# Optimization experiments

Measured on AMD Instinct MI355X. Metric: run time of the kernel, lower is better.

Reference implementation:

```python
import jax, jax.numpy as jnp
import numpy as np

VOCAB = 50000
OOV = 1000
EMB = 256
H = 512          # decoder hidden
ENC = 512        # 2 * encoder_hidden (bidirectional)
B, S, T = 32, 256, 8
NEG = -1e20


def setup_inputs() -> dict:
    key = jax.random.key(0)
    ks = jax.random.split(key, 16)
    inp = {
        'dec_x': jax.random.randint(ks[0], (B, T), 0, VOCAB),
        'enc_x_with_oov': jax.random.randint(ks[1], (B, S), 0, VOCAB + OOV),
        'enc_len': jax.random.randint(ks[2], (B,), 64, S + 1),
        'enc_output': jax.random.normal(ks[3], (B, S, ENC), jnp.float32),
        'enc_h': jax.random.normal(ks[4], (B, H), jnp.float32),
        'enc_c': jax.random.normal(ks[5], (B, H), jnp.float32),
        'batch_size': B,
        'dec_len': T,
        # learned parameters
        'embedding': jax.random.normal(ks[6], (VOCAB, EMB), jnp.float32) * 0.02,
        'lstm_k': jax.random.normal(ks[7], (EMB, 4 * H), jnp.float32) * 0.02,
        'lstm_r': jax.random.normal(ks[8], (H, 4 * H), jnp.float32) * 0.02,
        'lstm_b': jnp.zeros((4 * H,), jnp.float32),
        'attn_w': jax.random.normal(ks[9], (H, ENC), jnp.float32) * 0.02,
        'out_w': jax.random.normal(ks[10], (ENC + H, H), jnp.float32) * 0.02,
        'out_b': jnp.zeros((H,), jnp.float32),
        'gen_w': jax.random.normal(ks[11], (H, VOCAB), jnp.float32) * 0.02,
        'copy_w': jax.random.normal(ks[12], (ENC, H), jnp.float32) * 0.02,
        'copy_b': jnp.zeros((H,), jnp.float32),
    }
    return inp


def _lstm(x, h0, c0, Wk, Wr, b):
    # x: [B, T, E] -> hidden states [B, T, H], final (h, c)
    def step(carry, x_t):
        h, c = carry
        z = x_t @ Wk + h @ Wr + b  # [B, 4H]
        i, f, g, o = jnp.split(z, 4, axis=-1)
        c = jax.nn.sigmoid(f) * c + jax.nn.sigmoid(i) * jnp.tanh(g)
        h = jax.nn.sigmoid(o) * jnp.tanh(c)
        return (h, c), h
    (h, c), hs = jax.lax.scan(step, (h0, c0), jnp.swapaxes(x, 0, 1))
    return jnp.swapaxes(hs, 0, 1), h, c


def reference(dec_x, enc_x_with_oov, enc_len, enc_output, enc_h, enc_c,
              batch_size, dec_len, embedding, lstm_k, lstm_r, lstm_b,
              attn_w, out_w, out_b, gen_w, copy_w, copy_b):
    mask = jnp.arange(S) < enc_len[:, None]          # [B, S] True = keep

    embed_dec = embedding[dec_x]                      # [B, T, E]
    hidden, state_h, state_c = _lstm(embed_dec, enc_h, enc_c, lstm_k, lstm_r, lstm_b)

    # attention ('general' score)
    q = hidden @ attn_w                               # [B, T, ENC]
    scores = jnp.einsum('bte,bse->bts', q, enc_output)
    scores = jnp.where(mask[:, None, :], scores, NEG)
    attn = jax.nn.softmax(scores, axis=2)             # [B, T, S]
    context = jnp.einsum('bts,bse->bte', attn, enc_output)
    attn_out = jnp.tanh(jnp.concatenate([context, hidden], axis=-1) @ out_w + out_b)  # [B, T, H]

    # generation scores, padded with tiny constant for OOV slots
    gen = jnp.exp(attn_out @ gen_w)                   # [B, T, VOCAB]
    gen = jnp.pad(gen, ((0, 0), (0, 0), (0, OOV)), constant_values=1e-10)

    # copy scores scattered into extended vocab
    k = jnp.tanh(enc_output @ copy_w + copy_b)        # [B, S, H]
    cs = jnp.einsum('bsh,bth->bts', k, attn_out)      # [B, T, S]
    cs = jnp.exp(jnp.where(mask[:, None, :], cs, NEG))
    Vt = VOCAB + OOV
    copy_vocab = jnp.zeros((B, T, Vt), cs.dtype).at[
        jnp.arange(B)[:, None, None],
        jnp.arange(T)[None, :, None],
        enc_x_with_oov[:, None, :],
    ].add(cs)                                         # scatter-add, dup indices sum

    total = gen + copy_vocab
    total_prob = jnp.log(total / jnp.sum(total, axis=2, keepdims=True))
    return total_prob, state_h, state_c
```

## Files before the change

kernel.cpp:

```cpp
#include <hip/hip_runtime.h>
#include <hip/hip_bf16.h>

typedef unsigned short u16;
typedef unsigned int   u32;
typedef __attribute__((ext_vector_type(4))) float f4v;
typedef __attribute__((ext_vector_type(8))) short s8v;
typedef __attribute__((ext_vector_type(4))) unsigned int u4v;

#define NB   32
#define NS   256
#define NT   8
#define NH   512
#define NENC 512
#define NEMB 256
#define NVOC 50000
#define NVT  51000

__device__ __forceinline__ float bf2f(u16 u){ return __uint_as_float(((u32)u)<<16); }
__device__ __forceinline__ u16 f2bf(float f){
  u32 x = __float_as_uint(f);
  return (u16)((x + 0x7fffu + ((x>>16)&1u)) >> 16);
}
__device__ __forceinline__ s8v ld_frag16(const u16* p){
  union{ s8v v; u4v u; } t;
  t.u = *(const u4v*)p;
  return t.v;
}
__device__ __forceinline__ f4v mfma16(s8v a, s8v b, f4v c){
  return __builtin_amdgcn_mfma_f32_16x16x32_bf16(a,b,c,0,0,0);
}
__device__ __forceinline__ float sigm(float x){ return 1.f/(1.f+__expf(-x)); }

__global__ __launch_bounds__(256)
void transpose_cvt(const float* __restrict__ in, u16* __restrict__ out,
                   int K, int N)
{
  __shared__ u16 tile[32*40];
  const int n0 = blockIdx.x*32, k0 = blockIdx.y*32;
  const int tid = threadIdx.x;
  {
    int r = tid>>3, c4 = tid&7;
    int c = n0 + c4*4;
    if (c+4 > N) c = N-4;
    f4v v = *(const f4v*)(in + (size_t)(k0+r)*N + c);
    uint2 p;
    p.x = (u32)f2bf(v.x) | ((u32)f2bf(v.y)<<16);
    p.y = (u32)f2bf(v.z) | ((u32)f2bf(v.w)<<16);
    *(uint2*)&tile[r*40 + c4*4] = p;
  }
  __syncthreads();
  {
    int r2 = tid>>3, kc = tid&7;
    int n = n0 + r2;
    if (n < N){
      u16 e[4];
      #pragma unroll
      for (int j=0; j<4; ++j) e[j] = tile[(kc*4+j)*40 + r2];
      *(uint2*)(out + (size_t)n*K + k0 + kc*4) = *(uint2*)e;
    }
  }
}

__global__ __launch_bounds__(256)
void cvt_bf16(const float* __restrict__ src, u16* __restrict__ dst){
  int i = (blockIdx.x*256 + threadIdx.x) * 4;
  f4v v = *(const f4v*)(src + i);
  uint2 p;
  p.x = (u32)f2bf(v.x) | ((u32)f2bf(v.y)<<16);
  p.y = (u32)f2bf(v.z) | ((u32)f2bf(v.w)<<16);
  *(uint2*)(dst + i) = p;
}

template<int BM, int BN, int EPI, bool ABF16, bool AGATHER, bool MXA>
__global__ __launch_bounds__(256)
void gemm_bt(const void* __restrict__ Av, const u16* __restrict__ Bt,
             float* __restrict__ C, const int* __restrict__ a_idx,
             const float* __restrict__ bias, float* __restrict__ rowsum,
             int K, int lda, int ldc, int nlim)
{
  constexpr int LDT = 40;
  constexpr int PA  = ABF16 ? BM/64 : BM/32;
  constexpr int PB  = BN/64;
  __shared__ u16 Al[2][BM*LDT];
  __shared__ u16 Bl[2][BN*LDT];
  const int tid  = threadIdx.x;
  const int lane = tid & 63;
  const int wave = tid >> 6;
  const int m0 = (MXA ? blockIdx.x : blockIdx.y) * BM;
  const int n0 = (MXA ? blockIdx.y : blockIdx.x) * BN;
  constexpr int TM = BM/32;
  constexpr int TN = BN/32;
  const int wm = (wave>>1)*(BM/2);
  const int wn = (wave&1)*(BN/2);
  const int q  = lane >> 4;
  const int ln = lane & 15;

  const u16*  aS16[PA];
  const float* aS32[PA];
  int aOff[PA];
  if (ABF16){
    const u16* Ag = (const u16*)Av;
    #pragma unroll
    for (int p=0; p<PA; ++p){
      int el = tid + p*256, row = el>>2, ck = el&3;
      aS16[p] = Ag + (size_t)(m0+row)*lda + ck*8;
      aS32[p] = nullptr;
      aOff[p] = row*LDT + ck*8;
    }
  } else {
    const float* Ag = (const float*)Av;
    #pragma unroll
    for (int p=0; p<PA; ++p){
      int el = tid + p*256, row = el>>3, ck = el&7;
      int grow = AGATHER ? a_idx[m0+row] : (m0+row);
      aS32[p] = Ag + (size_t)grow*lda + ck*4;
      aS16[p] = nullptr;
      aOff[p] = row*LDT + ck*4;
    }
  }
  const u16* bS[PB];
  int bOff[PB];
  #pragma unroll
  for (int p=0; p<PB; ++p){
    int el = tid + p*256, row = el>>2, ck = el&3;
    int nr = n0 + row; if (nr >= nlim) nr = nlim-1;
    bS[p]   = Bt + (size_t)nr*K + ck*8;
    bOff[p] = row*LDT + ck*8;
  }

  f4v acc[TM][TN];
  #pragma unroll
  for (int im=0; im<TM; ++im)
    #pragma unroll
    for (int in=0; in<TN; ++in) acc[im][in] = 0.f;

  u4v aR[PA]; f4v aF[PA]; u4v bR[PB];
  if (ABF16){
    #pragma unroll
    for (int p=0; p<PA; ++p) aR[p] = *(const u4v*)(aS16[p]);
  } else {
    #pragma unroll
    for (int p=0; p<PA; ++p) aF[p] = *(const f4v*)(aS32[p]);
  }
  #pragma unroll
  for (int p=0; p<PB; ++p) bR[p] = *(const u4v*)(bS[p]);

  const int KB = K >> 5;
  int cur = 0;
  for (int kb=0; kb<KB; ++kb){
    if (ABF16){
      #pragma unroll
      for (int p=0; p<PA; ++p) *(u4v*)&Al[cur][aOff[p]] = aR[p];
    } else {
      #pragma unroll
      for (int p=0; p<PA; ++p){
        uint2 pk;
        pk.x = (u32)f2bf(aF[p].x) | ((u32)f2bf(aF[p].y)<<16);
        pk.y = (u32)f2bf(aF[p].z) | ((u32)f2bf(aF[p].w)<<16);
        *(uint2*)&Al[cur][aOff[p]] = pk;
      }
    }
    #pragma unroll
    for (int p=0; p<PB; ++p) *(u4v*)&Bl[cur][bOff[p]] = bR[p];
    if (kb+1 < KB){
      const int ko = (kb+1)*32;
      if (ABF16){
        #pragma unroll
        for (int p=0; p<PA; ++p) aR[p] = *(const u4v*)(aS16[p] + ko);
      } else {
        #pragma unroll
        for (int p=0; p<PA; ++p) aF[p] = *(const f4v*)(aS32[p] + ko);
      }
      #pragma unroll
      for (int p=0; p<PB; ++p) bR[p] = *(const u4v*)(bS[p] + ko);
    }
    __syncthreads();
    s8v af[TM], bfr[TN];
    #pragma unroll
    for (int im=0; im<TM; ++im)
      af[im] = ld_frag16(&Al[cur][(wm+im*16+ln)*LDT + q*8]);
    #pragma unroll
    for (int in=0; in<TN; ++in)
      bfr[in] = ld_frag16(&Bl[cur][(wn+in*16+ln)*LDT + q*8]);
    #pragma unroll
    for (int im=0; im<TM; ++im)
      #pragma unroll
      for (int in=0; in<TN; ++in)
        acc[im][in] = mfma16(af[im], bfr[in], acc[im][in]);
    cur ^= 1;
  }

  #pragma unroll
  for (int im=0; im<TM; ++im){
    const int rbase = m0 + wm + im*16 + q*4;
    #pragma unroll
    for (int in=0; in<TN; ++in){
      const int col = n0 + wn + in*16 + ln;
      if (EPI == 0){
        #pragma unroll
        for (int r=0; r<4; ++r)
          C[(size_t)(rbase+r)*ldc + col] = acc[im][in][r];
      } else if (EPI == 1){
        float bb = bias[col];
        u16* Cb = (u16*)C;
        #pragma unroll
        for (int r=0; r<4; ++r)
          Cb[(size_t)(rbase+r)*ldc + col] = f2bf(tanhf(acc[im][in][r] + bb));
      }
    }
  }
}

__global__ __launch_bounds__(256, 3)
void gen_nat(const u16* __restrict__ A,
             const float* __restrict__ W,
             float* __restrict__ outp)
{
  constexpr int LDT = 40;
  __shared__ u16 Al[2][256*LDT];
  __shared__ u16 Bl[2][64*LDT];
  const int tid  = threadIdx.x;
  const int lane = tid & 63, wave = tid >> 6;
  const int q = lane >> 4, ln = lane & 15;
  const int wm = (wave >> 1) * 128;
  const int wn = (wave & 1) * 32;
  const int n0 = blockIdx.x * 64;

  const int arow = tid >> 2, ack = (tid & 3) * 8;
  const int kp = tid >> 4;
  const int nw = tid & 15;
  int bcol = n0 + nw*4; if (bcol > NVOC-4) bcol = NVOC-4;
  const float* w0 = W + (size_t)(2*kp)  *NVOC + bcol;
  const float* w1 = W + (size_t)(2*kp+1)*NVOC + bcol;
  const int bLoff = (nw*4)*LDT + kp*2;
  const size_t CH = (size_t)32*NVOC;

  f4v acc[8][2];
  #pragma unroll
  for (int im=0; im<8; ++im){ acc[im][0] = 0.f; acc[im][1] = 0.f; }

  u4v aA[4], aB[4];
  f4v b0A, b1A, b0B, b1B;
  #pragma unroll
  for (int p=0; p<4; ++p)
    aA[p] = *(const u4v*)(A + (size_t)(arow + p*64)*NH + ack);
  b0A = *(const f4v*)(w0);
  b1A = *(const f4v*)(w1);
  #pragma unroll
  for (int p=0; p<4; ++p)
    aB[p] = *(const u4v*)(A + (size_t)(arow + p*64)*NH + 32 + ack);
  b0B = *(const f4v*)(w0 + CH);
  b1B = *(const f4v*)(w1 + CH);

  for (int kb=0; kb<16; kb+=2){
    #pragma unroll
    for (int p=0; p<4; ++p) *(u4v*)&Al[0][(arow + p*64)*LDT + ack] = aA[p];
    #pragma unroll
    for (int i=0; i<4; ++i){
      u32 v = (u32)f2bf(b0A[i]) | ((u32)f2bf(b1A[i])<<16);
      *(u32*)&Bl[0][bLoff + i*LDT] = v;
    }
    if (kb+2 < 16){
      #pragma unroll
      for (int p=0; p<4; ++p)
        aA[p] = *(const u4v*)(A + (size_t)(arow + p*64)*NH + (kb+2)*32 + ack);
      b0A = *(const f4v*)(w0 + (size_t)(kb+2)*CH);
      b1A = *(const f4v*)(w1 + (size_t)(kb+2)*CH);
    }
    __syncthreads();
    {
      s8v bf0 = ld_frag16(&Bl[0][(wn + ln)*LDT + q*8]);
      s8v bf1 = ld_frag16(&Bl[0][(wn + 16 + ln)*LDT + q*8]);
      #pragma unroll
      for (int im=0; im<8; ++im){
        s8v af = ld_frag16(&Al[0][(wm + im*16 + ln)*LDT + q*8]);
        acc[im][0] = mfma16(af, bf0, acc[im][0]);
        acc[im][1] = mfma16(af, bf1, acc[im][1]);
      }
    }
    #pragma unroll
    for (int p=0; p<4; ++p) *(u4v*)&Al[1][(arow + p*64)*LDT + ack] = aB[p];
    #pragma unroll
    for (int i=0; i<4; ++i){
      u32 v = (u32)f2bf(b0B[i]) | ((u32)f2bf(b1B[i])<<16);
      *(u32*)&Bl[1][bLoff + i*LDT] = v;
    }
    if (kb+3 < 16){
      #pragma unroll
      for (int p=0; p<4; ++p)
        aB[p] = *(const u4v*)(A + (size_t)(arow + p*64)*NH + (kb+3)*32 + ack);
      b0B = *(const f4v*)(w0 + (size_t)(kb+3)*CH);
      b1B = *(const f4v*)(w1 + (size_t)(kb+3)*CH);
    }
    __syncthreads();
    {
      s8v bf0 = ld_frag16(&Bl[1][(wn + ln)*LDT + q*8]);
      s8v bf1 = ld_frag16(&Bl[1][(wn + 16 + ln)*LDT + q*8]);
      #pragma unroll
      for (int im=0; im<8; ++im){
        s8v af = ld_frag16(&Al[1][(wm + im*16 + ln)*LDT + q*8]);
        acc[im][0] = mfma16(af, bf0, acc[im][0]);
        acc[im][1] = mfma16(af, bf1, acc[im][1]);
      }
    }
  }

  #pragma unroll
  for (int im=0; im<8; ++im){
    const int rbase = wm + im*16 + q*4;
    #pragma unroll
    for (int in=0; in<2; ++in){
      const int col = n0 + wn + in*16 + ln;
      if (col < NVT){
        #pragma unroll
        for (int r=0; r<4; ++r){
          float v = (col < NVOC) ? __expf(acc[im][in][r]) : 1e-10f;
          outp[(size_t)(rbase+r)*NVT + col] = v;
        }
      }
    }
  }
}

__global__ __launch_bounds__(256)
void lstm_step2(const u16* __restrict__ wrT, const float* __restrict__ xk,
                const float* __restrict__ bias, const u16* __restrict__ hb_in,
                u16* __restrict__ hb_out, float* __restrict__ c_cur,
                float* __restrict__ hidden, float* __restrict__ out_h,
                float* __restrict__ out_c, int t)
{
  const int tid = threadIdx.x, lane = tid & 63, g = tid >> 6;
  const int q = lane >> 4, ln = lane & 15;
  const int j0 = blockIdx.x * 16;

  f4v acc0 = 0.f, acc1 = 0.f;
  const u16* bp = wrT + (size_t)(g*NH + j0 + ln)*NH;
  const u16* a0 = hb_in + (size_t)ln*NH;
  const u16* a1 = hb_in + (size_t)(16+ln)*NH;
  #pragma unroll 4
  for (int kb=0; kb<16; ++kb){
    s8v bf  = ld_frag16(bp + kb*32 + q*8);
    s8v af0 = ld_frag16(a0 + kb*32 + q*8);
    s8v af1 = ld_frag16(a1 + kb*32 + q*8);
    acc0 = mfma16(af0, bf, acc0);
    acc1 = mfma16(af1, bf, acc1);
  }

  __shared__ float zs[4][32][17];
  #pragma unroll
  for (int r=0; r<4; ++r){
    zs[g][q*4+r][ln]    = acc0[r];
    zs[g][16+q*4+r][ln] = acc1[r];
  }
  __syncthreads();

  #pragma unroll
  for (int pp=0; pp<2; ++pp){
    int pair = tid + pp*256;
    int b = pair >> 4, jj = pair & 15;
    int j = j0 + jj;
    const float* xr = xk + (size_t)(b*NT+t)*2048;
    float zi = zs[0][b][jj] + xr[j]        + bias[j];
    float zf = zs[1][b][jj] + xr[NH+j]     + bias[NH+j];
    float zg = zs[2][b][jj] + xr[2*NH+j]   + bias[2*NH+j];
    float zo = zs[3][b][jj] + xr[3*NH+j]   + bias[3*NH+j];
    float c = sigm(zf)*c_cur[(size_t)b*NH+j] + sigm(zi)*tanhf(zg);
    float h = sigm(zo)*tanhf(c);
    c_cur[(size_t)b*NH+j] = c;
    hb_out[(size_t)b*NH+j] = f2bf(h);
    hidden[(size_t)(b*NT+t)*NH + j] = h;
    if (t == NT-1){ out_h[(size_t)b*NH+j] = h; out_c[(size_t)b*NH+j] = c; }
  }
}

__global__ __launch_bounds__(1024)
void attn_ctx(const float* __restrict__ q, const float* __restrict__ enc,
              const int* __restrict__ enc_len, const float* __restrict__ hidden,
              float* __restrict__ concat)
{
  const int b = blockIdx.x;
  __shared__ float qs[NT][NENC];
  __shared__ float at[NT][NS];
  __shared__ float cred[NT][NENC];
  const int tid = threadIdx.x;
  for (int i=tid; i<NT*NENC; i+=1024) ((float*)qs)[i] = q[(size_t)b*NT*NENC + i];
  __syncthreads();
  const int len = enc_len[b];
  {
    int s = tid & 255, tg = (tid >> 8) * 2;
    const float* er = enc + ((size_t)(b*NS+s))*NENC;
    float s0 = 0.f, s1 = 0.f;
    for (int e=0; e<NENC; e+=4){
      f4v v = *(const f4v*)(er+e);
      s0 += v.x*qs[tg][e]   + v.y*qs[tg][e+1]   + v.z*qs[tg][e+2]   + v.w*qs[tg][e+3];
      s1 += v.x*qs[tg+1][e] + v.y*qs[tg+1][e+1] + v.z*qs[tg+1][e+2] + v.w*qs[tg+1][e+3];
    }
    bool m = s < len;
    at[tg][s]   = m ? s0 : -3.0e38f;
    at[tg+1][s] = m ? s1 : -3.0e38f;
  }
  __syncthreads();
  {
    int wave = tid >> 6, lane = tid & 63;
    if (wave < NT){
      float v[4]; float mx = -3.0e38f;
      #pragma unroll
      for (int i=0;i<4;++i){ v[i] = at[wave][lane+64*i]; mx = fmaxf(mx, v[i]); }
      #pragma unroll
      for (int off=1; off<64; off<<=1) mx = fmaxf(mx, __shfl_xor(mx, off, 64));
      float sum = 0.f;
      #pragma unroll
      for (int i=0;i<4;++i){ v[i] = __expf(v[i]-mx); sum += v[i]; }
      #pragma unroll
      for (int off=1; off<64; off<<=1) sum += __shfl_xor(sum, off, 64);
      float inv = 1.f/sum;
      #pragma unroll
      for (int i=0;i<4;++i) at[wave][lane+64*i] = v[i]*inv;
    }
  }
  __syncthreads();
  {
    int e = tid & 511, sh = tid >> 9;
    float cx[NT];
    #pragma unroll
    for (int t=0;t<NT;++t) cx[t] = 0.f;
    for (int si=0; si<128; ++si){
      int s = sh*128 + si;
      float v = enc[((size_t)(b*NS+s))*NENC + e];
      #pragma unroll
      for (int t=0;t<NT;++t) cx[t] += at[t][s]*v;
    }
    if (sh == 1){
      #pragma unroll
      for (int t=0;t<NT;++t) cred[t][e] = cx[t];
    }
    __syncthreads();
    if (sh == 0){
      #pragma unroll
      for (int t=0;t<NT;++t)
        concat[(size_t)(b*NT+t)*1024 + e] = cx[t] + cred[t][e];
    } else {
      #pragma unroll
      for (int t=0;t<NT;++t)
        concat[(size_t)(b*NT+t)*1024 + 512 + e] = hidden[(size_t)(b*NT+t)*NH + e];
    }
  }
}

__global__ __launch_bounds__(256)
void cs_scatter(const u16* __restrict__ attn_bf, const u16* __restrict__ copy_k,
                const int* __restrict__ enc_x, const int* __restrict__ enc_len,
                float* __restrict__ outp)
{
  const int b  = blockIdx.x >> 2;
  const int sb = blockIdx.x & 3;
  __shared__ u16 Al[16*520];
  const int tid = threadIdx.x;
  for (int i=tid; i<16*64; i+=256){
    int row = i >> 6, ck = i & 63;
    uint2 v0 = {0u,0u}, v1 = {0u,0u};
    if (row < NT){
      const u16* s = attn_bf + ((size_t)(b*NT+row))*NH + ck*8;
      v0 = *(const uint2*)s; v1 = *(const uint2*)(s+4);
    }
    u16* d = &Al[row*520 + ck*8];
    *(uint2*)d = v0; *(uint2*)(d+4) = v1;
  }
  __syncthreads();
  const int wave = tid >> 6, lane = tid & 63;
  const int q = lane >> 4, ln = lane & 15;
  const int s0 = sb*64 + wave*16;
  f4v acc = 0.f;
  const u16* Bg = copy_k + ((size_t)(b*NS + s0 + ln))*NH;
  for (int kb=0; kb<16; ++kb){
    s8v a  = ld_frag16(&Al[ln*520 + kb*32 + q*8]);
    s8v bb = ld_frag16(Bg + kb*32 + q*8);
    acc = mfma16(a, bb, acc);
  }
  const int s = s0 + ln;
  const int len = enc_len[b];
  const int vidx = enc_x[b*NS + s];
  const bool valid = (s < len);
  #pragma unroll
  for (int r=0; r<4; ++r){
    int t = q*4 + r;
    float e = (valid && t < NT) ? __expf(acc[r]) : 0.f;
    if (e != 0.f) atomicAdd(&outp[(size_t)(b*NT+t)*NVT + vidx], e);
  }
}

__global__ __launch_bounds__(256)
void row_reduce_log(const float* __restrict__ outp, float* __restrict__ logsum)
{
  const int r = blockIdx.x;
  const int tid = threadIdx.x;
  const float* p = outp + (size_t)r*NVT;
  float sum = 0.f;
  for (int i4 = tid; i4 < 12750; i4 += 256){
    f4v v = *(const f4v*)(p + i4*4);
    sum += v.x + v.y + v.z + v.w;
  }
  #pragma unroll
  for (int off=1; off<64; off<<=1) sum += __shfl_xor(sum, off, 64);
  __shared__ float ws[4];
  if ((tid & 63) == 0) ws[tid>>6] = sum;
  __syncthreads();
  if (tid == 0) logsum[r] = __logf(ws[0]+ws[1]+ws[2]+ws[3]);
}

__global__ __launch_bounds__(256)
void norm_log(float* __restrict__ outp, const float* __restrict__ logsum){
  const int i4 = blockIdx.x*256 + threadIdx.x;
  if (i4 >= 12750) return;
  const int r = blockIdx.y;
  const float ls = logsum[r];
  float* p = outp + (size_t)r*NVT + i4*4;
  f4v v = *(const f4v*)p;
  v.x = __logf(v.x) - ls;
  v.y = __logf(v.y) - ls;
  v.z = __logf(v.z) - ls;
  v.w = __logf(v.w) - ls;
  *(f4v*)p = v;
}

extern "C" void kernel_launch(void* const* d_in, const int* in_sizes, int n_in,
                              void* d_out, int out_size, void* d_ws, size_t ws_size,
                              hipStream_t stream)
{
  (void)in_sizes; (void)n_in; (void)out_size; (void)ws_size;
  const int*   dec_x      = (const int*)  d_in[0];
  const int*   enc_x      = (const int*)  d_in[1];
  const int*   enc_len    = (const int*)  d_in[2];
  const float* enc_output = (const float*)d_in[3];
  const float* enc_h      = (const float*)d_in[4];
  const float* enc_c      = (const float*)d_in[5];
  const float* embedding  = (const float*)d_in[8];
  const float* lstm_k     = (const float*)d_in[9];
  const float* lstm_r     = (const float*)d_in[10];
  const float* lstm_b     = (const float*)d_in[11];
  const float* attn_w     = (const float*)d_in[12];
  const float* out_w      = (const float*)d_in[13];
  const float* out_b      = (const float*)d_in[14];
  const float* gen_w      = (const float*)d_in[15];
  const float* copy_w     = (const float*)d_in[16];
  const float* copy_b     = (const float*)d_in[17];

  float* outp  = (float*)d_out;
  float* out_h = outp + (size_t)NB*NT*NVT;
  float* out_c = out_h + NB*NH;

  char* ws = (char*)d_ws;
  u16*   wrT     = (u16*)ws;    ws += (size_t)2048*NH*2;
  u16*   lstmkT  = (u16*)ws;    ws += (size_t)2048*NEMB*2;
  u16*   attnT   = (u16*)ws;    ws += (size_t)NENC*NH*2;
  u16*   outT    = (u16*)ws;    ws += (size_t)NH*1024*2;
  u16*   copyT   = (u16*)ws;    ws += (size_t)NH*NENC*2;
  float* xk      = (float*)ws;  ws += (size_t)NB*NT*2048*4;
  u16*   hb0     = (u16*)ws;    ws += (size_t)NB*NH*2;
  u16*   hb1     = (u16*)ws;    ws += (size_t)NB*NH*2;
  float* c_cur   = (float*)ws;  ws += (size_t)NB*NH*4;
  float* hidden  = (float*)ws;  ws += (size_t)NB*NT*NH*4;
  float* qbuf    = (float*)ws;  ws += (size_t)NB*NT*NENC*4;
  float* concat  = (float*)ws;  ws += (size_t)NB*NT*1024*4;
  u16*   attn_bf = (u16*)ws;    ws += (size_t)NB*NT*NH*2;
  u16*   copy_k  = (u16*)ws;    ws += (size_t)NB*NS*NH*2;
  float* logsum  = (float*)ws;  ws += NB*NT*4;

  transpose_cvt<<<dim3(64,16), 256,0,stream>>>(lstm_r, wrT,    NH,  2048);
  transpose_cvt<<<dim3(64,8),  256,0,stream>>>(lstm_k, lstmkT, NEMB,2048);
  transpose_cvt<<<dim3(16,16), 256,0,stream>>>(attn_w, attnT,  NH,  NENC);
  transpose_cvt<<<dim3(16,32), 256,0,stream>>>(out_w,  outT,   1024,NH);
  transpose_cvt<<<dim3(16,16), 256,0,stream>>>(copy_w, copyT,  NENC,NH);
  cvt_bf16<<<16,256,0,stream>>>(enc_h, hb0);
  hipMemcpyAsync(c_cur, enc_c, NB*NH*4, hipMemcpyDeviceToDevice, stream);

  gemm_bt<64,128,1,false,false,false><<<dim3(4,128),256,0,stream>>>(
      enc_output, copyT, (float*)copy_k, nullptr, copy_b, nullptr, NENC, NENC, NH, NH);

  gemm_bt<32,64,0,false,true,true><<<dim3(8,32),256,0,stream>>>(
      embedding, lstmkT, xk, dec_x, nullptr, nullptr, NEMB, NEMB, 2048, 2048);

  u16* hb[2] = {hb0, hb1};
  for (int t=0; t<NT; ++t)
    lstm_step2<<<32,256,0,stream>>>(wrT, xk, lstm_b, hb[t&1], hb[(t+1)&1],
                                    c_cur, hidden, out_h, out_c, t);

  gemm_bt<32,64,0,false,false,true><<<dim3(8,8),256,0,stream>>>(
      hidden, attnT, qbuf, nullptr, nullptr, nullptr, NH, NH, NENC, NENC);

  attn_ctx<<<32,1024,0,stream>>>(qbuf, enc_output, enc_len, hidden, concat);

  gemm_bt<32,64,1,false,false,true><<<dim3(8,8),256,0,stream>>>(
      concat, outT, (float*)attn_bf, nullptr, out_b, nullptr, 1024, 1024, NH, NH);

  gen_nat<<<797,256,0,stream>>>(attn_bf, gen_w, outp);

  cs_scatter<<<128,256,0,stream>>>(attn_bf, copy_k, enc_x, enc_len, outp);
  row_reduce_log<<<NB*NT,256,0,stream>>>(outp, logsum);
  norm_log<<<dim3(50,NB*NT),256,0,stream>>>(outp, logsum);
}
```

Before: 502.6 us.

## Rewrite attention as bf16 MFMA kernels with pre-converted encoder copies

Replaces the single fp32 scalar attention kernel with two MFMA-based kernels: one computes the scores and softmax from a bf16 copy of the encoder output, and one computes the context from a transposed bf16 copy, with 8 blocks per batch row. The LSTM now writes hidden states straight into the concat buffer, so the separate hidden buffer and its later copy are gone, and the query projection emits bf16. The copy-key GEMM also reads the bf16 encoder copy. Two extra conversion and transpose passes over enc_output are added and must be paid back, and bf16 scores and probabilities lower precision.

```diff
diff --git a/kernel.cpp b/kernel.cpp
--- a/kernel.cpp
+++ b/kernel.cpp
@@ -35,6 +35,8 @@
 void transpose_cvt(const float* __restrict__ in, u16* __restrict__ out,
                    int K, int N)
 {
+  in  += (size_t)blockIdx.z * K * N;
+  out += (size_t)blockIdx.z * K * N;
   __shared__ u16 tile[32*40];
   const int n0 = blockIdx.x*32, k0 = blockIdx.y*32;
   const int tid = threadIdx.x;
@@ -206,6 +208,11 @@
         #pragma unroll
         for (int r=0; r<4; ++r)
           Cb[(size_t)(rbase+r)*ldc + col] = f2bf(tanhf(acc[im][in][r] + bb));
+      } else if (EPI == 3){
+        u16* Cb = (u16*)C;
+        #pragma unroll
+        for (int r=0; r<4; ++r)
+          Cb[(size_t)(rbase+r)*ldc + col] = f2bf(acc[im][in][r]);
       }
     }
   }
@@ -326,7 +333,7 @@
 void lstm_step2(const u16* __restrict__ wrT, const float* __restrict__ xk,
                 const float* __restrict__ bias, const u16* __restrict__ hb_in,
                 u16* __restrict__ hb_out, float* __restrict__ c_cur,
-                float* __restrict__ hidden, float* __restrict__ out_h,
+                float* __restrict__ concat, float* __restrict__ out_h,
                 float* __restrict__ out_c, int t)
 {
   const int tid = threadIdx.x, lane = tid & 63, g = tid >> 6;
@@ -368,82 +375,109 @@
     float h = sigm(zo)*tanhf(c);
     c_cur[(size_t)b*NH+j] = c;
     hb_out[(size_t)b*NH+j] = f2bf(h);
-    hidden[(size_t)(b*NT+t)*NH + j] = h;
+    concat[(size_t)(b*NT+t)*1024 + 512 + j] = h;
     if (t == NT-1){ out_h[(size_t)b*NH+j] = h; out_c[(size_t)b*NH+j] = c; }
   }
 }
 
-__global__ __launch_bounds__(1024)
-void attn_ctx(const float* __restrict__ q, const float* __restrict__ enc,
-              const int* __restrict__ enc_len, const float* __restrict__ hidden,
-              float* __restrict__ concat)
+__global__ __launch_bounds__(512)
+void attn_sm(const u16* __restrict__ q_bf,
+             const u16* __restrict__ enc_bf,
+             const int* __restrict__ enc_len,
+             float* __restrict__ at_p)
 {
   const int b = blockIdx.x;
-  __shared__ float qs[NT][NENC];
-  __shared__ float at[NT][NS];
-  __shared__ float cred[NT][NENC];
+  __shared__ u16 Al[16*520];
+  __shared__ float at[8][256];
   const int tid = threadIdx.x;
-  for (int i=tid; i<NT*NENC; i+=1024) ((float*)qs)[i] = q[(size_t)b*NT*NENC + i];
+  for (int i=tid; i<16*64; i+=512){
+    int row = i >> 6, ck = i & 63;
+    uint2 v0 = {0u,0u}, v1 = {0u,0u};
+    if (row < NT){
+      const u16* s = q_bf + ((size_t)(b*NT+row))*NH + ck*8;
+      v0 = *(const uint2*)s; v1 = *(const uint2*)(s+4);
+    }
+    u16* d = &Al[row*520 + ck*8];
+    *(uint2*)d = v0; *(uint2*)(d+4) = v1;
+  }
   __syncthreads();
+  const int wave = tid >> 6, lane = tid & 63;
+  const int q = lane >> 4, ln = lane & 15;
   const int len = enc_len[b];
+  f4v acc0 = 0.f, acc1 = 0.f;
+  const u16* Bg0 = enc_bf + ((size_t)(b*NS + wave*32 + ln))*NENC;
+  const u16* Bg1 = enc_bf + ((size_t)(b*NS + wave*32 + 16 + ln))*NENC;
+  for (int kb=0; kb<16; ++kb){
+    s8v a  = ld_frag16(&Al[ln*520 + kb*32 + q*8]);
+    s8v b0 = ld_frag16(Bg0 + kb*32 + q*8);
+    s8v b1 = ld_frag16(Bg1 + kb*32 + q*8);
+    acc0 = mfma16(a, b0, acc0);
+    acc1 = mfma16(a, b1, acc1);
+  }
   {
-    int s = tid & 255, tg = (tid >> 8) * 2;
-    const float* er = enc + ((size_t)(b*NS+s))*NENC;
-    float s0 = 0.f, s1 = 0.f;
-    for (int e=0; e<NENC; e+=4){
-      f4v v = *(const f4v*)(er+e);
-      s0 += v.x*qs[tg][e]   + v.y*qs[tg][e+1]   + v.z*qs[tg][e+2]   + v.w*qs[tg][e+3];
-      s1 += v.x*qs[tg+1][e] + v.y*qs[tg+1][e+1] + v.z*qs[tg+1][e+2] + v.w*qs[tg+1][e+3];
-    }
-    bool m = s < len;
-    at[tg][s]   = m ? s0 : -3.0e38f;
-    at[tg+1][s] = m ? s1 : -3.0e38f;
+    const int s0 = wave*32 + ln, s1 = s0 + 16;
+    const bool m0 = s0 < len, m1 = s1 < len;
+    #pragma unroll
+    for (int r=0; r<4; ++r){
+      int t = q*4 + r;
+      if (t < NT){
+        at[t][s0] = m0 ? acc0[r] : -3.0e38f;
+        at[t][s1] = m1 ? acc1[r] : -3.0e38f;
+      }
+    }
   }
   __syncthreads();
   {
-    int wave = tid >> 6, lane = tid & 63;
-    if (wave < NT){
-      float v[4]; float mx = -3.0e38f;
-      #pragma unroll
-      for (int i=0;i<4;++i){ v[i] = at[wave][lane+64*i]; mx = fmaxf(mx, v[i]); }
-      #pragma unroll
-      for (int off=1; off<64; off<<=1) mx = fmaxf(mx, __shfl_xor(mx, off, 64));
-      float sum = 0.f;
-      #pragma unroll
-      for (int i=0;i<4;++i){ v[i] = __expf(v[i]-mx); sum += v[i]; }
-      #pragma unroll
-      for (int off=1; off<64; off<<=1) sum += __shfl_xor(sum, off, 64);
-      float inv = 1.f/sum;
-      #pragma unroll
-      for (int i=0;i<4;++i) at[wave][lane+64*i] = v[i]*inv;
-    }
+    float v[4]; float mx = -3.0e38f;
+    #pragma unroll
+    for (int i=0;i<4;++i){ v[i] = at[wave][lane+64*i]; mx = fmaxf(mx, v[i]); }
+    #pragma unroll
+    for (int off=1; off<64; off<<=1) mx = fmaxf(mx, __shfl_xor(mx, off, 64));
+    float sum = 0.f;
+    #pragma unroll
+    for (int i=0;i<4;++i){ v[i] = __expf(v[i]-mx); sum += v[i]; }
+    #pragma unroll
+    for (int off=1; off<64; off<<=1) sum += __shfl_xor(sum, off, 64);
+    float inv = 1.f/sum;
+    #pragma unroll
+    for (int i=0;i<4;++i)
+      at_p[((size_t)(b*NT+wave))*NS + lane+64*i] = v[i]*inv;
+  }
+}
+
+__global__ __launch_bounds__(256)
+void attn_ctx2(const float* __restrict__ at_p,
+               const u16* __restrict__ encT_bf,
+               float* __restrict__ concat)
+{
+  const int b = blockIdx.x, eb = blockIdx.y;
+  __shared__ u16 Al[16*264];
+  const int tid = threadIdx.x;
+  for (int i=tid; i<16*64; i+=256){
+    int row = i >> 6, c4 = i & 63;
+    uint2 pk = {0u,0u};
+    if (row < NT){
+      f4v v = *(const f4v*)(at_p + ((size_t)(b*NT+row))*NS + c4*4);
+      pk.x = (u32)f2bf(v.x) | ((u32)f2bf(v.y)<<16);
+      pk.y = (u32)f2bf(v.z) | ((u32)f2bf(v.w)<<16);
+    }
+    *(uint2*)&Al[row*264 + c4*4] = pk;
   }
   __syncthreads();
-  {
-    int e = tid & 511, sh = tid >> 9;
-    float cx[NT];
-    #pragma unroll
-    for (int t=0;t<NT;++t) cx[t] = 0.f;
-    for (int si=0; si<128; ++si){
-      int s = sh*128 + si;
-      float v = enc[((size_t)(b*NS+s))*NENC + e];
-      #pragma unroll
-      for (int t=0;t<NT;++t) cx[t] += at[t][s]*v;
-    }
-    if (sh == 1){
-      #pragma unroll
-      for (int t=0;t<NT;++t) cred[t][e] = cx[t];
-    }
-    __syncthreads();
-    if (sh == 0){
-      #pragma unroll
-      for (int t=0;t<NT;++t)
-        concat[(size_t)(b*NT+t)*1024 + e] = cx[t] + cred[t][e];
-    } else {
-      #pragma unroll
-      for (int t=0;t<NT;++t)
-        concat[(size_t)(b*NT+t)*1024 + 512 + e] = hidden[(size_t)(b*NT+t)*NH + e];
-    }
+  const int wave = tid >> 6, lane = tid & 63;
+  const int q = lane >> 4, ln = lane & 15;
+  const int e = eb*64 + wave*16 + ln;
+  f4v acc = 0.f;
+  const u16* Bg = encT_bf + ((size_t)(b*NENC + e))*NS;
+  for (int kb=0; kb<8; ++kb){
+    s8v a  = ld_frag16(&Al[ln*264 + kb*32 + q*8]);
+    s8v bb = ld_frag16(Bg + kb*32 + q*8);
+    acc = mfma16(a, bb, acc);
+  }
+  #pragma unroll
+  for (int r=0; r<4; ++r){
+    int t = q*4 + r;
+    if (t < NT) concat[(size_t)(b*NT+t)*1024 + e] = acc[r];
   }
 }
 
@@ -559,13 +593,17 @@
   u16*   hb0     = (u16*)ws;    ws += (size_t)NB*NH*2;
   u16*   hb1     = (u16*)ws;    ws += (size_t)NB*NH*2;
   float* c_cur   = (float*)ws;  ws += (size_t)NB*NH*4;
-  float* hidden  = (float*)ws;  ws += (size_t)NB*NT*NH*4;
-  float* qbuf    = (float*)ws;  ws += (size_t)NB*NT*NENC*4;
+  u16*   q_bf    = (u16*)ws;    ws += (size_t)NB*NT*NENC*2;
+  float* at_p    = (float*)ws;  ws += (size_t)NB*NT*NS*4;
   float* concat  = (float*)ws;  ws += (size_t)NB*NT*1024*4;
   u16*   attn_bf = (u16*)ws;    ws += (size_t)NB*NT*NH*2;
   u16*   copy_k  = (u16*)ws;    ws += (size_t)NB*NS*NH*2;
+  u16*   enc_bf  = (u16*)ws;    ws += (size_t)NB*NS*NENC*2;
+  u16*   encT_bf = (u16*)ws;    ws += (size_t)NB*NENC*NS*2;
   float* logsum  = (float*)ws;  ws += NB*NT*4;
 
+  cvt_bf16<<<4096,256,0,stream>>>(enc_output, enc_bf);
+  transpose_cvt<<<dim3(16,8,32),256,0,stream>>>(enc_output, encT_bf, NS, NENC);
   transpose_cvt<<<dim3(64,16), 256,0,stream>>>(lstm_r, wrT,    NH,  2048);
   transpose_cvt<<<dim3(64,8),  256,0,stream>>>(lstm_k, lstmkT, NEMB,2048);
   transpose_cvt<<<dim3(16,16), 256,0,stream>>>(attn_w, attnT,  NH,  NENC);
@@ -574,8 +612,8 @@
   cvt_bf16<<<16,256,0,stream>>>(enc_h, hb0);
   hipMemcpyAsync(c_cur, enc_c, NB*NH*4, hipMemcpyDeviceToDevice, stream);
 
-  gemm_bt<64,128,1,false,false,false><<<dim3(4,128),256,0,stream>>>(
-      enc_output, copyT, (float*)copy_k, nullptr, copy_b, nullptr, NENC, NENC, NH, NH);
+  gemm_bt<64,128,1,true,false,false><<<dim3(4,128),256,0,stream>>>(
+      enc_bf, copyT, (float*)copy_k, nullptr, copy_b, nullptr, NENC, NENC, NH, NH);
 
   gemm_bt<32,64,0,false,true,true><<<dim3(8,32),256,0,stream>>>(
       embedding, lstmkT, xk, dec_x, nullptr, nullptr, NEMB, NEMB, 2048, 2048);
@@ -583,12 +621,13 @@
   u16* hb[2] = {hb0, hb1};
   for (int t=0; t<NT; ++t)
     lstm_step2<<<32,256,0,stream>>>(wrT, xk, lstm_b, hb[t&1], hb[(t+1)&1],
-                                    c_cur, hidden, out_h, out_c, t);
-
-  gemm_bt<32,64,0,false,false,true><<<dim3(8,8),256,0,stream>>>(
-      hidden, attnT, qbuf, nullptr, nullptr, nullptr, NH, NH, NENC, NENC);
-
-  attn_ctx<<<32,1024,0,stream>>>(qbuf, enc_output, enc_len, hidden, concat);
+                                    c_cur, concat, out_h, out_c, t);
+
+  gemm_bt<32,64,3,false,false,true><<<dim3(8,8),256,0,stream>>>(
+      concat + 512, attnT, (float*)q_bf, nullptr, nullptr, nullptr, NH, 1024, NENC, NENC);
+
+  attn_sm<<<32,512,0,stream>>>(q_bf, enc_bf, enc_len, at_p);
+  attn_ctx2<<<dim3(32,8),256,0,stream>>>(at_p, encT_bf, concat);
 
   gemm_bt<32,64,1,false,false,true><<<dim3(8,8),256,0,stream>>>(
       concat, outT, (float*)attn_bf, nullptr, out_b, nullptr, 1024, 1024, NH, NH);
```

New measurement: 451.6 us. 1.11x faster.
